# Performance work log

Hardware: AMD Instinct MI355X
Metric: run time of the kernel (lower is better)

The kernel has to match this reference:

```python
import jax, jax.numpy as jnp
import numpy as np

ALPHA = 0.25
GAMMA = 2.0
MARGIN = 1.0
LAMBDA_GRAPH = 0.1
N = 8192
D = 128


def setup_inputs() -> dict:
    key = jax.random.key(0)
    k1, k2, k3, k4 = jax.random.split(key, 4)
    preds = jax.random.normal(k1, (N,), dtype=jnp.float32)
    targets = jax.random.randint(k2, (N,), 0, 2).astype(jnp.float32)  # binary labels
    features = jax.random.normal(k3, (N, D), dtype=jnp.float32)
    graph_features = jax.random.normal(k4, (N, D), dtype=jnp.float32)
    return {"preds": preds, "targets": targets, "features": features,
            "graph_features": graph_features}


def _focal_loss(preds, targets):
    # numerically stable BCE-with-logits, reduction='none'
    bce = jnp.maximum(preds, 0.0) - preds * targets + jnp.log1p(jnp.exp(-jnp.abs(preds)))
    pt = jnp.exp(-bce)
    return jnp.mean(ALPHA * (1.0 - pt) ** GAMMA * bce)


def _contrastive_loss(features, labels):
    # squared pairwise distances via ||a||^2 + ||b||^2 - 2 a.b  -> [N, N]
    sqn = jnp.sum(features * features, axis=-1)
    sq = sqn[:, None] + sqn[None, :] - 2.0 * (features @ features.T)
    sq = jnp.maximum(sq, 0.0)
    # safe sqrt (gradient-safe at 0)
    pos = sq > 0.0
    dist = jnp.where(pos, jnp.sqrt(jnp.where(pos, sq, 1.0)), 0.0)
    same = labels[:, None] == labels[None, :]
    # same-label pairs: dist^2 == sq ; different: clamp(margin - dist, 0)^2
    per_pair = jnp.where(same, sq, jnp.maximum(MARGIN - dist, 0.0) ** 2)
    return jnp.mean(per_pair)  # sum / N^2


def _graph_reg_loss(graph_features):
    diff = graph_features[1:] - graph_features[:-1]
    return jnp.mean(jnp.sqrt(jnp.sum(diff * diff, axis=1)))


def reference(preds, targets, features, graph_features):
    return (_focal_loss(preds, targets)
            + _contrastive_loss(features, targets)
            + LAMBDA_GRAPH * _graph_reg_loss(graph_features))
```

## Files before the change

kernel.cpp:

```cpp
#include <hip/hip_runtime.h>
#include <hip/hip_bf16.h>


#define N_PTS 8192
#define DIM 128

typedef __bf16 bf16x8 __attribute__((ext_vector_type(8)));
typedef float f32x4 __attribute__((ext_vector_type(4)));

#define VPART_OFF 0
#define SPART_OFF (128 * 256 * 4)
#define CTRL_OFF  (SPART_OFF + 128 * 16)

#define NPAIR 2080
#define NFOCAL 32
#define NGRAPH 256
#define TOTAL_BLOCKS (NPAIR + NFOCAL + NGRAPH + 1)

__device__ __forceinline__ bf16x8 pack8(const float4 a, const float4 b) {
    bf16x8 r;
    r[0] = (__bf16)a.x; r[1] = (__bf16)a.y; r[2] = (__bf16)a.z; r[3] = (__bf16)a.w;
    r[4] = (__bf16)b.x; r[5] = (__bf16)b.y; r[6] = (__bf16)b.z; r[7] = (__bf16)b.w;
    return r;
}
__device__ __forceinline__ float ssq8(const float4 a, const float4 b) {
    return a.x * a.x + a.y * a.y + a.z * a.z + a.w * a.w
         + b.x * b.x + b.y * b.y + b.z * b.z + b.w * b.w;
}

__global__ __launch_bounds__(256) void prep_kernel(const float* __restrict__ feat,
                                                   const float* __restrict__ targets,
                                                   float* __restrict__ vpart,
                                                   float* __restrict__ spart,
                                                   unsigned long long* __restrict__ ctrl) {
    const int b = blockIdx.x;
    const int tid = threadIdx.x;
    if (b == 128) {
        if (tid == 0) {
            *reinterpret_cast<unsigned*>(ctrl) = 0u;
            double* a = reinterpret_cast<double*>(ctrl);
            a[1] = 0.0; a[2] = 0.0; a[3] = 0.0;
        }
        return;
    }
    __shared__ float fA[512], f1[512];
    __shared__ float sred[4][3];
    const int w = tid >> 6, lane = tid & 63;
    const float2* feat2 = reinterpret_cast<const float2*>(feat);
    float2 accA = {0.f, 0.f}, acc1 = {0.f, 0.f};
    float ssqA = 0.f, ssq1 = 0.f, n1 = 0.f;
    int r = b * 64 + w * 16;
    #pragma unroll 4
    for (int i = 0; i < 16; ++i, ++r) {
        const float2 v = feat2[r * 64 + lane];
        const float tr = targets[r];
        accA.x += v.x; accA.y += v.y;
        acc1.x += tr * v.x; acc1.y += tr * v.y;
        const float s2 = v.x * v.x + v.y * v.y;
        ssqA += s2; ssq1 += tr * s2; n1 += tr;
    }
    fA[w * 128 + 2 * lane] = accA.x; fA[w * 128 + 2 * lane + 1] = accA.y;
    f1[w * 128 + 2 * lane] = acc1.x; f1[w * 128 + 2 * lane + 1] = acc1.y;
    #pragma unroll
    for (int off = 32; off > 0; off >>= 1) {
        ssqA += __shfl_down(ssqA, off);
        ssq1 += __shfl_down(ssq1, off);
    }
    if (lane == 0) { sred[w][0] = ssqA; sred[w][1] = ssq1; sred[w][2] = n1; }
    __syncthreads();
    if (tid < 128) {
        const int d = tid;
        const float c1 = f1[d] + f1[128 + d] + f1[256 + d] + f1[384 + d];
        const float ca = fA[d] + fA[128 + d] + fA[256 + d] + fA[384 + d];
        vpart[b * 256 + tid] = ca - c1;
    } else {
        const int d = tid - 128;
        vpart[b * 256 + tid] = f1[d] + f1[128 + d] + f1[256 + d] + f1[384 + d];
    }
    if (tid == 0) {
        float4 s;
        s.x = sred[0][0] + sred[1][0] + sred[2][0] + sred[3][0];
        s.y = sred[0][1] + sred[1][1] + sred[2][1] + sred[3][1];
        s.z = sred[0][2] + sred[1][2] + sred[2][2] + sred[3][2];
        s.w = 0.f;
        *reinterpret_cast<float4*>(spart + b * 4) = s;
    }
}

template<bool DIAG>
__device__ __forceinline__ float scan_slow(const f32x4 (&acc)[4][4],
                                           const f32x4 (&sqni)[4], const f32x4 (&ti4)[4],
                                           const float (&sqnj)[4], const float (&tj4)[4],
                                           int wm, int wn, int quad, int m15) {
    float lsum = 0.f;
    #pragma unroll
    for (int tm = 0; tm < 4; ++tm) {
        #pragma unroll
        for (int tn = 0; tn < 4; ++tn) {
            const int jl = wn * 64 + tn * 16 + m15;
            #pragma unroll
            for (int e = 0; e < 4; ++e) {
                const float sq = sqni[tm][e] + sqnj[tn] - 2.f * acc[tm][tn][e];
                bool excl = (ti4[tm][e] == tj4[tn]);
                if (DIAG) {
                    const int il = wm * 64 + tm * 16 + quad * 4 + e;
                    excl = excl || (jl <= il);
                }
                if (!excl && sq < 1.f) {
                    const float d = sqrtf(fmaxf(sq, 0.f));
                    const float m = 1.f - d;
                    lsum += 2.f * m * m;
                }
            }
        }
    }
    return lsum;
}

__global__ __launch_bounds__(256, 4) void main_kernel(const float* __restrict__ feat,
                                                      const float* __restrict__ preds,
                                                      const float* __restrict__ targets,
                                                      const float* __restrict__ gfeat,
                                                      const float* __restrict__ vpart,
                                                      const float* __restrict__ spart,
                                                      unsigned* __restrict__ counter,
                                                      double* __restrict__ accs,
                                                      float* __restrict__ out) {
    __shared__ __align__(16) float smem[1024];
    const int bx = blockIdx.x;
    const int tid = threadIdx.x;
    const int w = tid >> 6, lane = tid & 63;
    double addv = 0.0;
    int acc_idx = 1;

    if (bx < NPAIR) {
        const int u = bx;
        const int vv = 2079 - u;
        int k = (int)((sqrtf(8.f * (float)vv + 1.f) - 1.f) * 0.5f);
        while ((k + 1) * (k + 2) / 2 <= vv) ++k;
        while (k * (k + 1) / 2 > vv) --k;
        const int bi = 63 - k;
        const int bj = 63 - (vv - k * (k + 1) / 2);

        const int quad = lane >> 4, m15 = lane & 15;
        const int wm = w >> 1, wn = w & 1;
        const int ibase = bi * 128 + wm * 64, jbase = bj * 128 + wn * 64;

        bf16x8 afs[4], bfs[4];
        float sA[4], sB[4];
        #pragma unroll
        for (int t = 0; t < 4; ++t) {
            const float* pa = feat + (ibase + t * 16 + m15) * DIM + 8 * quad;
            const float4 a0 = *reinterpret_cast<const float4*>(pa);
            const float4 a1 = *reinterpret_cast<const float4*>(pa + 4);
            afs[t] = pack8(a0, a1);
            float s = ssq8(a0, a1);
            s += __shfl_xor(s, 16); s += __shfl_xor(s, 32);
            sA[t] = s;
            const float* pb = feat + (jbase + t * 16 + m15) * DIM + 8 * quad;
            const float4 b0 = *reinterpret_cast<const float4*>(pb);
            const float4 b1 = *reinterpret_cast<const float4*>(pb + 4);
            bfs[t] = pack8(b0, b1);
            float sb = ssq8(b0, b1);
            sb += __shfl_xor(sb, 16); sb += __shfl_xor(sb, 32);
            sB[t] = sb;
        }
        f32x4 acc[4][4];
        #pragma unroll
        for (int a = 0; a < 4; ++a)
            #pragma unroll
            for (int b = 0; b < 4; ++b) acc[a][b] = (f32x4){0.f, 0.f, 0.f, 0.f};
        #pragma unroll
        for (int tm = 0; tm < 4; ++tm)
            #pragma unroll
            for (int tn = 0; tn < 4; ++tn)
                acc[tm][tn] = __builtin_amdgcn_mfma_f32_16x16x32_bf16(
                    afs[tm], bfs[tn], acc[tm][tn], 0, 0, 0);

        float minv = 1e30f;
        #pragma unroll
        for (int tm = 0; tm < 4; ++tm) {
            #pragma unroll
            for (int e = 0; e < 4; ++e) {
                const float sa = __shfl(sA[tm], quad * 4 + e);
                #pragma unroll
                for (int tn = 0; tn < 4; ++tn)
                    minv = fminf(minv, sa + sB[tn] - 2.f * acc[tm][tn][e]);
            }
        }

        float lsum = 0.f;
        if (__any(minv < 2.f)) {
            float qi = 0.f, qj = 0.f;
            {
                const float4* ri = reinterpret_cast<const float4*>(feat + (ibase + lane) * DIM);
                const float4* rj = reinterpret_cast<const float4*>(feat + (jbase + lane) * DIM);
                #pragma unroll 8
                for (int c2 = 0; c2 < 32; ++c2) {
                    const float4 x = ri[c2]; qi += x.x * x.x + x.y * x.y + x.z * x.z + x.w * x.w;
                    const float4 y = rj[c2]; qj += y.x * y.x + y.y * y.y + y.z * y.z + y.w * y.w;
                }
            }
            f32x4 sqni[4], ti4[4];
            float sqnj[4], tj4[4];
            #pragma unroll
            for (int tm = 0; tm < 4; ++tm) {
                #pragma unroll
                for (int e = 0; e < 4; ++e) sqni[tm][e] = __shfl(qi, tm * 16 + quad * 4 + e);
                ti4[tm] = *reinterpret_cast<const f32x4*>(targets + ibase + tm * 16 + quad * 4);
            }
            #pragma unroll
            for (int tn = 0; tn < 4; ++tn) {
                sqnj[tn] = __shfl(qj, tn * 16 + m15);
                tj4[tn] = targets[jbase + tn * 16 + m15];
            }
            for (int ks = 1; ks < 4; ++ks) {
                bf16x8 af2[4], bf2[4];
                #pragma unroll
                for (int t = 0; t < 4; ++t) {
                    const float* pa = feat + (ibase + t * 16 + m15) * DIM + 8 * (quad + 4 * ks);
                    af2[t] = pack8(*reinterpret_cast<const float4*>(pa),
                                   *reinterpret_cast<const float4*>(pa + 4));
                    const float* pb = feat + (jbase + t * 16 + m15) * DIM + 8 * (quad + 4 * ks);
                    bf2[t] = pack8(*reinterpret_cast<const float4*>(pb),
                                   *reinterpret_cast<const float4*>(pb + 4));
                }
                #pragma unroll
                for (int tm = 0; tm < 4; ++tm)
                    #pragma unroll
                    for (int tn = 0; tn < 4; ++tn)
                        acc[tm][tn] = __builtin_amdgcn_mfma_f32_16x16x32_bf16(
                            af2[tm], bf2[tn], acc[tm][tn], 0, 0, 0);
            }
            lsum = (bi == bj)
                ? scan_slow<true >(acc, sqni, ti4, sqnj, tj4, wm, wn, quad, m15)
                : scan_slow<false>(acc, sqni, ti4, sqnj, tj4, wm, wn, quad, m15);
            #pragma unroll
            for (int off = 32; off > 0; off >>= 1) lsum += __shfl_down(lsum, off);
        }
        if (lane == 0) smem[w] = lsum;
        __syncthreads();
        if (tid == 0) {
            addv = (double)(smem[0] + smem[1] + smem[2] + smem[3]);
            acc_idx = 1;
        }
    } else if (bx < NPAIR + NFOCAL) {
        const int b = bx - NPAIR;
        const int i = b * 256 + tid;
        const float p = preds[i], t = targets[i];
        const float bce = fmaxf(p, 0.f) - p * t + log1pf(expf(-fabsf(p)));
        const float pt = expf(-bce);
        const float om = 1.f - pt;
        float fv = 0.25f * om * om * bce;
        #pragma unroll
        for (int off = 32; off > 0; off >>= 1) fv += __shfl_down(fv, off);
        if (lane == 0) smem[w] = fv;
        __syncthreads();
        if (tid == 0) {
            addv = (double)(smem[0] + smem[1] + smem[2] + smem[3]);
            acc_idx = 2;
        }
    } else if (bx < NPAIR + NFOCAL + NGRAPH) {
        const int b = bx - NPAIR - NFOCAL;
        float ga = 0.f;
        #pragma unroll
        for (int it = 0; it < 8; ++it) {
            const int r = b * 4 + w + it * 1024;
            if (r < N_PTS - 1) {
                const float2 a = *reinterpret_cast<const float2*>(gfeat + r * DIM + lane * 2);
                const float2 bb = *reinterpret_cast<const float2*>(gfeat + (r + 1) * DIM + lane * 2);
                const float dx = bb.x - a.x, dy = bb.y - a.y;
                float s = dx * dx + dy * dy;
                #pragma unroll
                for (int off = 32; off > 0; off >>= 1) s += __shfl_down(s, off);
                if (lane == 0) ga += sqrtf(s);
            }
        }
        if (lane == 0) smem[w] = ga;
        __syncthreads();
        if (tid == 0) {
            addv = (double)(smem[0] + smem[1] + smem[2] + smem[3]);
            acc_idx = 3;
        }
    } else {
        float V = 0.f;
        #pragma unroll 8
        for (int b2 = 0; b2 < 128; ++b2) V += vpart[b2 * 256 + tid];
        double vsq = (double)V * (double)V;
        #pragma unroll
        for (int off = 32; off > 0; off >>= 1) vsq += __shfl_down(vsq, off);
        double* dred = reinterpret_cast<double*>(smem);
        if (lane == 0) dred[w] = vsq;
        double st = 0.0, s1 = 0.0, n1 = 0.0;
        if (tid < 128) {
            const float4 s = *reinterpret_cast<const float4*>(spart + tid * 4);
            st = s.x; s1 = s.y; n1 = s.z;
        }
        #pragma unroll
        for (int off = 32; off > 0; off >>= 1) {
            st += __shfl_down(st, off);
            s1 += __shfl_down(s1, off);
            n1 += __shfl_down(n1, off);
        }
        if (lane == 0) { dred[4 + w * 3] = st; dred[5 + w * 3] = s1; dred[6 + w * 3] = n1; }
        __syncthreads();
        if (tid == 0) {
            const double v0sq = dred[0] + dred[1];
            const double v1sq = dred[2] + dred[3];
            const double stot = dred[4] + dred[7];
            const double s1s  = dred[5] + dred[8];
            const double n1s  = dred[6] + dred[9];
            const double n0s = (double)N_PTS - n1s;
            const double s0s = stot - s1s;
            addv = 2.0 * (n0s * s0s - v0sq) + 2.0 * (n1s * s1s - v1sq);
            acc_idx = 1;
        }
    }

    if (tid == 0) {
        if (addv != 0.0) {
            atomicAdd(accs + acc_idx, addv);
            asm volatile("s_waitcnt vmcnt(0)" ::: "memory");
        }
        const unsigned old = atomicAdd(counter, 1u);
        if (old == TOTAL_BLOCKS - 1) {
            const double c = atomicAdd(accs + 1, 0.0);
            const double f = atomicAdd(accs + 2, 0.0);
            const double g = atomicAdd(accs + 3, 0.0);
            out[0] = (float)(c / ((double)N_PTS * (double)N_PTS)
                             + f / (double)N_PTS
                             + 0.1 * (g / (double)(N_PTS - 1)));
        }
    }
}

extern "C" void kernel_launch(void* const* d_in, const int* in_sizes, int n_in,
                              void* d_out, int out_size, void* d_ws, size_t ws_size,
                              hipStream_t stream) {
    const float* preds    = (const float*)d_in[0];
    const float* targets  = (const float*)d_in[1];
    const float* features = (const float*)d_in[2];
    const float* gfeat    = (const float*)d_in[3];
    char* ws = (char*)d_ws;
    float* vpart = (float*)(ws + VPART_OFF);
    float* spart = (float*)(ws + SPART_OFF);
    unsigned long long* ctrl = (unsigned long long*)(ws + CTRL_OFF);

    prep_kernel<<<129, 256, 0, stream>>>(features, targets, vpart, spart, ctrl);
    main_kernel<<<TOTAL_BLOCKS, 256, 0, stream>>>(features, preds, targets, gfeat,
                                                  vpart, spart,
                                                  (unsigned*)ctrl, (double*)ctrl,
                                                  (float*)d_out);
}
```

Before: 121.5 us.

## Replace atomic last-block reduction with per-wave partials and finalize kernel

```diff
diff --git a/kernel.cpp b/kernel.cpp
--- a/kernel.cpp
+++ b/kernel.cpp
@@ -9,13 +9,15 @@
 typedef float f32x4 __attribute__((ext_vector_type(4)));
 
 #define VPART_OFF 0
-#define SPART_OFF (128 * 256 * 4)
-#define CTRL_OFF  (SPART_OFF + 128 * 16)
+#define SPART_OFF 131072
+#define CPART_OFF 133120
+#define FPART_OFF 166400
+#define GPART_OFF 166912
 
 #define NPAIR 2080
 #define NFOCAL 32
 #define NGRAPH 256
-#define TOTAL_BLOCKS (NPAIR + NFOCAL + NGRAPH + 1)
+#define NMAIN (NPAIR + NFOCAL + NGRAPH)
 
 __device__ __forceinline__ bf16x8 pack8(const float4 a, const float4 b) {
     bf16x8 r;
@@ -31,18 +33,9 @@
 __global__ __launch_bounds__(256) void prep_kernel(const float* __restrict__ feat,
                                                    const float* __restrict__ targets,
                                                    float* __restrict__ vpart,
-                                                   float* __restrict__ spart,
-                                                   unsigned long long* __restrict__ ctrl) {
+                                                   float* __restrict__ spart) {
     const int b = blockIdx.x;
     const int tid = threadIdx.x;
-    if (b == 128) {
-        if (tid == 0) {
-            *reinterpret_cast<unsigned*>(ctrl) = 0u;
-            double* a = reinterpret_cast<double*>(ctrl);
-            a[1] = 0.0; a[2] = 0.0; a[3] = 0.0;
-        }
-        return;
-    }
     __shared__ float fA[512], f1[512];
     __shared__ float sred[4][3];
     const int w = tid >> 6, lane = tid & 63;
@@ -121,17 +114,12 @@
                                                       const float* __restrict__ preds,
                                                       const float* __restrict__ targets,
                                                       const float* __restrict__ gfeat,
-                                                      const float* __restrict__ vpart,
-                                                      const float* __restrict__ spart,
-                                                      unsigned* __restrict__ counter,
-                                                      double* __restrict__ accs,
-                                                      float* __restrict__ out) {
-    __shared__ __align__(16) float smem[1024];
+                                                      float* __restrict__ c_part,
+                                                      float* __restrict__ f_part,
+                                                      float* __restrict__ g_part) {
     const int bx = blockIdx.x;
     const int tid = threadIdx.x;
     const int w = tid >> 6, lane = tid & 63;
-    double addv = 0.0;
-    int acc_idx = 1;
 
     if (bx < NPAIR) {
         const int u = bx;
@@ -238,12 +226,7 @@
             #pragma unroll
             for (int off = 32; off > 0; off >>= 1) lsum += __shfl_down(lsum, off);
         }
-        if (lane == 0) smem[w] = lsum;
-        __syncthreads();
-        if (tid == 0) {
-            addv = (double)(smem[0] + smem[1] + smem[2] + smem[3]);
-            acc_idx = 1;
-        }
+        if (lane == 0) c_part[u * 4 + w] = lsum;
     } else if (bx < NPAIR + NFOCAL) {
         const int b = bx - NPAIR;
         const int i = b * 256 + tid;
@@ -254,13 +237,8 @@
         float fv = 0.25f * om * om * bce;
         #pragma unroll
         for (int off = 32; off > 0; off >>= 1) fv += __shfl_down(fv, off);
-        if (lane == 0) smem[w] = fv;
-        __syncthreads();
-        if (tid == 0) {
-            addv = (double)(smem[0] + smem[1] + smem[2] + smem[3]);
-            acc_idx = 2;
-        }
-    } else if (bx < NPAIR + NFOCAL + NGRAPH) {
+        if (lane == 0) f_part[b * 4 + w] = fv;
+    } else {
         const int b = bx - NPAIR - NFOCAL;
         float ga = 0.f;
         #pragma unroll
@@ -276,61 +254,66 @@
                 if (lane == 0) ga += sqrtf(s);
             }
         }
-        if (lane == 0) smem[w] = ga;
-        __syncthreads();
-        if (tid == 0) {
-            addv = (double)(smem[0] + smem[1] + smem[2] + smem[3]);
-            acc_idx = 3;
-        }
-    } else {
-        float V = 0.f;
-        #pragma unroll 8
-        for (int b2 = 0; b2 < 128; ++b2) V += vpart[b2 * 256 + tid];
-        double vsq = (double)V * (double)V;
-        #pragma unroll
-        for (int off = 32; off > 0; off >>= 1) vsq += __shfl_down(vsq, off);
-        double* dred = reinterpret_cast<double*>(smem);
-        if (lane == 0) dred[w] = vsq;
-        double st = 0.0, s1 = 0.0, n1 = 0.0;
-        if (tid < 128) {
-            const float4 s = *reinterpret_cast<const float4*>(spart + tid * 4);
-            st = s.x; s1 = s.y; n1 = s.z;
-        }
-        #pragma unroll
-        for (int off = 32; off > 0; off >>= 1) {
-            st += __shfl_down(st, off);
-            s1 += __shfl_down(s1, off);
-            n1 += __shfl_down(n1, off);
-        }
-        if (lane == 0) { dred[4 + w * 3] = st; dred[5 + w * 3] = s1; dred[6 + w * 3] = n1; }
-        __syncthreads();
-        if (tid == 0) {
-            const double v0sq = dred[0] + dred[1];
-            const double v1sq = dred[2] + dred[3];
-            const double stot = dred[4] + dred[7];
-            const double s1s  = dred[5] + dred[8];
-            const double n1s  = dred[6] + dred[9];
-            const double n0s = (double)N_PTS - n1s;
-            const double s0s = stot - s1s;
-            addv = 2.0 * (n0s * s0s - v0sq) + 2.0 * (n1s * s1s - v1sq);
-            acc_idx = 1;
-        }
-    }
-
+        if (lane == 0) g_part[b * 4 + w] = ga;
+    }
+}
+
+__global__ __launch_bounds__(256) void finalize_kernel(const float* __restrict__ c_part,
+                                                       const float* __restrict__ f_part,
+                                                       const float* __restrict__ g_part,
+                                                       const float* __restrict__ vpart,
+                                                       const float* __restrict__ spart,
+                                                       float* __restrict__ out) {
+    __shared__ double sC[4], sF[4], sG[4], sV[4], sST[4], sS1[4], sN1[4];
+    const int tid = threadIdx.x;
+    const int w = tid >> 6, lane = tid & 63;
+
+    double c = 0.0;
+    for (int i = tid; i < NPAIR * 4; i += 256) c += (double)c_part[i];
+    double f = (tid < NFOCAL * 4) ? (double)f_part[tid] : 0.0;
+    double g = 0.0;
+    for (int i = tid; i < NGRAPH * 4; i += 256) g += (double)g_part[i];
+
+    float V = 0.f;
+    #pragma unroll 8
+    for (int b2 = 0; b2 < 128; ++b2) V += vpart[b2 * 256 + tid];
+    double vsq = (double)V * (double)V;
+
+    double st = 0.0, s1 = 0.0, n1 = 0.0;
+    if (tid < 128) {
+        const float4 s = *reinterpret_cast<const float4*>(spart + tid * 4);
+        st = s.x; s1 = s.y; n1 = s.z;
+    }
+    #pragma unroll
+    for (int off = 32; off > 0; off >>= 1) {
+        c += __shfl_down(c, off);
+        f += __shfl_down(f, off);
+        g += __shfl_down(g, off);
+        vsq += __shfl_down(vsq, off);
+        st += __shfl_down(st, off);
+        s1 += __shfl_down(s1, off);
+        n1 += __shfl_down(n1, off);
+    }
+    if (lane == 0) {
+        sC[w] = c; sF[w] = f; sG[w] = g; sV[w] = vsq;
+        sST[w] = st; sS1[w] = s1; sN1[w] = n1;
+    }
+    __syncthreads();
     if (tid == 0) {
-        if (addv != 0.0) {
-            atomicAdd(accs + acc_idx, addv);
-            asm volatile("s_waitcnt vmcnt(0)" ::: "memory");
-        }
-        const unsigned old = atomicAdd(counter, 1u);
-        if (old == TOTAL_BLOCKS - 1) {
-            const double c = atomicAdd(accs + 1, 0.0);
-            const double f = atomicAdd(accs + 2, 0.0);
-            const double g = atomicAdd(accs + 3, 0.0);
-            out[0] = (float)(c / ((double)N_PTS * (double)N_PTS)
-                             + f / (double)N_PTS
-                             + 0.1 * (g / (double)(N_PTS - 1)));
-        }
+        const double cs = sC[0] + sC[1] + sC[2] + sC[3];
+        const double fs = sF[0] + sF[1] + sF[2] + sF[3];
+        const double gs = sG[0] + sG[1] + sG[2] + sG[3];
+        const double v0sq = sV[0] + sV[1];
+        const double v1sq = sV[2] + sV[3];
+        const double stot = sST[0] + sST[1] + sST[2] + sST[3];
+        const double s1s  = sS1[0] + sS1[1] + sS1[2] + sS1[3];
+        const double n1s  = sN1[0] + sN1[1] + sN1[2] + sN1[3];
+        const double n0s = (double)N_PTS - n1s;
+        const double s0s = stot - s1s;
+        const double same = 2.0 * (n0s * s0s - v0sq) + 2.0 * (n1s * s1s - v1sq);
+        out[0] = (float)((cs + same) / ((double)N_PTS * (double)N_PTS)
+                         + fs / (double)N_PTS
+                         + 0.1 * (gs / (double)(N_PTS - 1)));
     }
 }
 
@@ -342,13 +325,15 @@
     const float* features = (const float*)d_in[2];
     const float* gfeat    = (const float*)d_in[3];
     char* ws = (char*)d_ws;
-    float* vpart = (float*)(ws + VPART_OFF);
-    float* spart = (float*)(ws + SPART_OFF);
-    unsigned long long* ctrl = (unsigned long long*)(ws + CTRL_OFF);
-
-    prep_kernel<<<129, 256, 0, stream>>>(features, targets, vpart, spart, ctrl);
-    main_kernel<<<TOTAL_BLOCKS, 256, 0, stream>>>(features, preds, targets, gfeat,
-                                                  vpart, spart,
-                                                  (unsigned*)ctrl, (double*)ctrl,
-                                                  (float*)d_out);
-}
+    float* vpart  = (float*)(ws + VPART_OFF);
+    float* spart  = (float*)(ws + SPART_OFF);
+    float* c_part = (float*)(ws + CPART_OFF);
+    float* f_part = (float*)(ws + FPART_OFF);
+    float* g_part = (float*)(ws + GPART_OFF);
+    float* out = (float*)d_out;
+
+    prep_kernel<<<128, 256, 0, stream>>>(features, targets, vpart, spart);
+    main_kernel<<<NMAIN, 256, 0, stream>>>(features, preds, targets, gfeat,
+                                           c_part, f_part, g_part);
+    finalize_kernel<<<1, 256, 0, stream>>>(c_part, f_part, g_part, vpart, spart, out);
+}
```

Result: no change. 123.8 us (+1.9%).
